# Optimization experiments

Hardware: AMD Instinct MI355X
Metric: run time of the kernel (lower is better)

## Reference

```python
import jax, jax.numpy as jnp
import numpy as np


def setup_inputs() -> dict:
    key = jax.random.key(0)
    ks = jax.random.split(key, 8)
    B, M, C, H, W = 2, 16, 256, 64, 64
    T = 1024  # transformer_dim
    return {
        "transformer_output": jax.random.normal(ks[0], (B, T), dtype=jnp.float32),
        "residual_maps": jax.random.normal(ks[1], (B, M, C, H, W), dtype=jnp.float32),
        "Wq": jax.random.normal(ks[2], (C, T), dtype=jnp.float32) * 0.02,
        "bq": jnp.zeros((C,), dtype=jnp.float32),
        "Wk": jax.random.normal(ks[3], (C, C), dtype=jnp.float32) * 0.02,
        "bk": jnp.zeros((C,), dtype=jnp.float32),
        "Wv": jax.random.normal(ks[4], (C, C), dtype=jnp.float32) * 0.02,
        "bv": jnp.zeros((C,), dtype=jnp.float32),
    }


def reference(transformer_output, residual_maps, Wq, bq, Wk, bk, Wv, bv):
    # residual_maps: [B, M, C, H, W]; single query per batch element.
    B, M, C, H, W = residual_maps.shape
    scale = C ** (-0.5)
    # Linear query projection: [B, C]
    q = transformer_output @ Wq.T + bq
    # 1x1 conv == per-pixel channel matmul: [B, M, C, H, W]
    keys = jnp.einsum("oc,bmchw->bmohw", Wk, residual_maps) + bk[None, None, :, None, None]
    values = jnp.einsum("oc,bmchw->bmohw", Wv, residual_maps) + bv[None, None, :, None, None]
    # Single-query dot-product scores per (map, pixel): [B, M, H, W]
    scores = jnp.einsum("bc,bmchw->bmhw", q, keys) * scale
    # Temporal softmax over num_maps at each spatial position
    probs = jax.nn.softmax(scores, axis=1)
    # Softmax-weighted sum of value maps: [B, C, H, W]
    out = jnp.einsum("bmhw,bmchw->bchw", probs, values)
    return out
```

## Files before the change

kernel.cpp:

```cpp
#include <hip/hip_runtime.h>

#define SCALE 0.0625f

typedef __attribute__((ext_vector_type(4))) float f32x4;
typedef __attribute__((ext_vector_type(8))) short s16x8;

__device__ __forceinline__ unsigned short f2bf(float x) {
    unsigned u = __float_as_uint(x);
    u = u + 0x7FFF + ((u >> 16) & 1);
    return (unsigned short)(u >> 16);
}

__global__ __launch_bounds__(256) void prep1_kernel(
    const float* __restrict__ TO,
    const float* __restrict__ Wq,
    const float* __restrict__ bq,
    const float* __restrict__ Wv,
    float* __restrict__ qbuf,
    unsigned short* __restrict__ WvB)
{
    const int blk = blockIdx.x;
    const int t   = threadIdx.x;
    if (blk < 16) {
        const int b    = blk >> 3;
        const int rblk = blk & 7;
        const int wv = t >> 6, l = t & 63;
        const float4* Wq4 = (const float4*)Wq;
        const float4* TO4 = (const float4*)TO;
        for (int rr = 0; rr < 8; ++rr) {
            const int c = rblk * 32 + wv * 8 + rr;
            float acc = 0.f;
#pragma unroll
            for (int i = 0; i < 4; ++i) {
                float4 wq = Wq4[c * 256 + i * 64 + l];
                float4 tv = TO4[b * 256 + i * 64 + l];
                acc = fmaf(wq.x, tv.x, acc);
                acc = fmaf(wq.y, tv.y, acc);
                acc = fmaf(wq.z, tv.z, acc);
                acc = fmaf(wq.w, tv.w, acc);
            }
#pragma unroll
            for (int mask = 1; mask < 64; mask <<= 1)
                acc += __shfl_xor(acc, mask, 64);
            if (l == 0) qbuf[b * 256 + c] = acc + bq[c];
        }
    } else {
        const int idx = blk - 16;
#pragma unroll
        for (int i = 0; i < 4; ++i) {
            const int e = idx * 4096 + i * 1024 + t * 4;
            const float4 f = ((const float4*)Wv)[e >> 2];
            ushort4 o;
            o.x = f2bf(f.x); o.y = f2bf(f.y);
            o.z = f2bf(f.z); o.w = f2bf(f.w);
            *(ushort4*)(WvB + e) = o;
        }
    }
}

__global__ __launch_bounds__(256) void prep2_kernel(
    const float* __restrict__ qbuf,
    const float* __restrict__ Wk,
    float* __restrict__ qks)
{
    const int blk = blockIdx.x;
    const int t   = threadIdx.x;
    const int b = blk >> 3, j = blk & 7;
    const int col = t & 31, chunk = t >> 5;
    const int cp = j * 32 + col;
    float partial = 0.f;
#pragma unroll 8
    for (int cc = 0; cc < 32; ++cc) {
        const int c = chunk * 32 + cc;
        partial = fmaf(qbuf[b * 256 + c], Wk[c * 256 + cp], partial);
    }
    __shared__ float r2[8][32];
    r2[chunk][col] = partial;
    __syncthreads();
    if (t < 32) {
        float s = 0.f;
#pragma unroll
        for (int k = 0; k < 8; ++k) s += r2[k][t];
        qks[b * 256 + j * 32 + t] = SCALE * s;
    }
}

__global__ __launch_bounds__(256) void scores_kernel(
    const float* __restrict__ X,
    const float* __restrict__ qks,
    float* __restrict__ scores)
{
    const int blk = blockIdx.x;
    const int bm  = blk >> 4;
    const int px  = ((blk & 15) << 8) + threadIdx.x;
    const float* __restrict__ Xr = X + bm * 1048576 + px;
    const float* __restrict__ qr = qks + (bm >> 4) * 256;
    float s0 = 0.f, s1 = 0.f, s2 = 0.f, s3 = 0.f;
#pragma unroll 4
    for (int c = 0; c < 256; c += 4) {
        s0 = fmaf(qr[c + 0], Xr[(c + 0) * 4096], s0);
        s1 = fmaf(qr[c + 1], Xr[(c + 1) * 4096], s1);
        s2 = fmaf(qr[c + 2], Xr[(c + 2) * 4096], s2);
        s3 = fmaf(qr[c + 3], Xr[(c + 3) * 4096], s3);
    }
    scores[bm * 4096 + px] = (s0 + s1) + (s2 + s3);
}

__global__ __launch_bounds__(256) void wxconv_kernel(
    const float* __restrict__ X,
    const float* __restrict__ scores,
    const unsigned short* __restrict__ WvB,
    const float* __restrict__ bv,
    float* __restrict__ out)
{
    const int t   = threadIdx.x;
    const int blk = blockIdx.x;
    const int pb  = ((blk & 7) << 6) | (blk >> 3);
    const int b   = pb >> 8;
    const int hw0 = (pb & 255) << 4;

    __shared__ float pl[16][16];
    __shared__ float invl[16];
    __shared__ float slab[256 * 20];

    {
        const int px_s = t & 15, m_s = t >> 4;
        const float e = __expf(scores[(b * 16 + m_s) * 4096 + hw0 + px_s]);
        pl[m_s][px_s] = e;
        __syncthreads();
        if (t < 16) {
            float s = 0.f;
#pragma unroll
            for (int m = 0; m < 16; ++m) s += pl[m][t];
            invl[t] = 1.0f / s;
        }
        __syncthreads();
        pl[m_s][px_s] *= invl[px_s];
        __syncthreads();
    }

    const int p4 = t & 3;
    const int cg = t >> 2;
    const float4* X4 = (const float4*)X;
    const int base0 = (b * 16) * 262144 + (hw0 >> 2) + p4;

    float4 v[2][4];
    float4 wx[4];
#pragma unroll
    for (int k = 0; k < 4; ++k) wx[k] = make_float4(0.f, 0.f, 0.f, 0.f);

#pragma unroll
    for (int k = 0; k < 4; ++k)
        v[0][k] = X4[base0 + (cg + 64 * k) * 1024];
    float4 pm[2];
    pm[0] = *(const float4*)&pl[0][4 * p4];

#pragma unroll
    for (int m = 0; m < 16; ++m) {
        const int buf = m & 1, nxt = buf ^ 1;
        if (m < 15) {
#pragma unroll
            for (int k = 0; k < 4; ++k)
                v[nxt][k] = X4[base0 + (m + 1) * 262144 + (cg + 64 * k) * 1024];
            pm[nxt] = *(const float4*)&pl[m + 1][4 * p4];
        }
#pragma unroll
        for (int k = 0; k < 4; ++k) {
            wx[k].x = fmaf(pm[buf].x, v[buf][k].x, wx[k].x);
            wx[k].y = fmaf(pm[buf].y, v[buf][k].y, wx[k].y);
            wx[k].z = fmaf(pm[buf].z, v[buf][k].z, wx[k].z);
            wx[k].w = fmaf(pm[buf].w, v[buf][k].w, wx[k].w);
        }
    }

#pragma unroll
    for (int k = 0; k < 4; ++k)
        *(float4*)&slab[(cg + 64 * k) * 20 + 4 * p4] = wx[k];
    __syncthreads();

    const int w    = t >> 6;
    const int lane = t & 63;
    const int px   = lane & 15;
    const int quad = lane >> 4;

    f32x4 acc[4];
#pragma unroll
    for (int i = 0; i < 4; ++i) {
        const int tt = 4 * w + i;
#pragma unroll
        for (int r = 0; r < 4; ++r)
            acc[i][r] = bv[16 * tt + quad * 4 + r];
    }

#pragma unroll
    for (int ks = 0; ks < 8; ++ks) {
        s16x8 bfr;
#pragma unroll
        for (int j = 0; j < 8; ++j)
            bfr[j] = (short)f2bf(slab[(ks * 32 + quad * 8 + j) * 20 + px]);
#pragma unroll
        for (int i = 0; i < 4; ++i) {
            const int tt = 4 * w + i;
            const s16x8 afr =
                *(const s16x8*)(WvB + (16 * tt + px) * 256 + ks * 32 + quad * 8);
            acc[i] = __builtin_amdgcn_mfma_f32_16x16x32_bf16(afr, bfr, acc[i],
                                                             0, 0, 0);
        }
    }

    const int obase = b * 1048576 + hw0;
#pragma unroll
    for (int i = 0; i < 4; ++i) {
        const int tt = 4 * w + i;
#pragma unroll
        for (int r = 0; r < 4; ++r) {
            const int co = 16 * tt + quad * 4 + r;
            out[obase + co * 4096 + px] = acc[i][r];
        }
    }
}

extern "C" void kernel_launch(void* const* d_in, const int* in_sizes, int n_in,
                              void* d_out, int out_size, void* d_ws, size_t ws_size,
                              hipStream_t stream) {
    const float* TO = (const float*)d_in[0];
    const float* X  = (const float*)d_in[1];
    const float* Wq = (const float*)d_in[2];
    const float* bq = (const float*)d_in[3];
    const float* Wk = (const float*)d_in[4];
    const float* Wv = (const float*)d_in[6];
    const float* bv = (const float*)d_in[7];
    float* out = (float*)d_out;
    float* ws  = (float*)d_ws;

    float*          qbuf   = ws;
    float*          qks    = ws + 512;
    unsigned short* WvB    = (unsigned short*)(ws + 1024);
    float*          scores = ws + 1024 + 32768;

    hipLaunchKernelGGL(prep1_kernel, dim3(32), dim3(256), 0, stream,
                       TO, Wq, bq, Wv, qbuf, WvB);
    hipLaunchKernelGGL(prep2_kernel, dim3(16), dim3(256), 0, stream,
                       qbuf, Wk, qks);
    hipLaunchKernelGGL(scores_kernel, dim3(512), dim3(256), 0, stream,
                       X, qks, scores);
    hipLaunchKernelGGL(wxconv_kernel, dim3(512), dim3(256), 0, stream,
                       X, scores, WvB, bv, out);
}
```

Baseline: 251.0 us.

## Fuse score computation into weighted-conv kernel with 32-pixel tiles

```diff
diff --git a/kernel.cpp b/kernel.cpp
--- a/kernel.cpp
+++ b/kernel.cpp
@@ -85,66 +85,59 @@
     }
 }
 
-__global__ __launch_bounds__(256) void scores_kernel(
+__global__ __launch_bounds__(512, 1) void fused_kernel(
     const float* __restrict__ X,
     const float* __restrict__ qks,
-    float* __restrict__ scores)
-{
-    const int blk = blockIdx.x;
-    const int bm  = blk >> 4;
-    const int px  = ((blk & 15) << 8) + threadIdx.x;
-    const float* __restrict__ Xr = X + bm * 1048576 + px;
-    const float* __restrict__ qr = qks + (bm >> 4) * 256;
-    float s0 = 0.f, s1 = 0.f, s2 = 0.f, s3 = 0.f;
-#pragma unroll 4
-    for (int c = 0; c < 256; c += 4) {
-        s0 = fmaf(qr[c + 0], Xr[(c + 0) * 4096], s0);
-        s1 = fmaf(qr[c + 1], Xr[(c + 1) * 4096], s1);
-        s2 = fmaf(qr[c + 2], Xr[(c + 2) * 4096], s2);
-        s3 = fmaf(qr[c + 3], Xr[(c + 3) * 4096], s3);
-    }
-    scores[bm * 4096 + px] = (s0 + s1) + (s2 + s3);
-}
-
-__global__ __launch_bounds__(256) void wxconv_kernel(
-    const float* __restrict__ X,
-    const float* __restrict__ scores,
     const unsigned short* __restrict__ WvB,
     const float* __restrict__ bv,
     float* __restrict__ out)
 {
     const int t   = threadIdx.x;
     const int blk = blockIdx.x;
-    const int pb  = ((blk & 7) << 6) | (blk >> 3);
-    const int b   = pb >> 8;
-    const int hw0 = (pb & 255) << 4;
-
-    __shared__ float pl[16][16];
-    __shared__ float invl[16];
-    __shared__ float slab[256 * 20];
+    const int b   = blk >> 7;
+    const int hw0 = (blk & 127) << 5;
+
+    __shared__ float pl[16][32];
+    __shared__ float invl[32];
+    __shared__ float slab[256 * 36];
 
     {
-        const int px_s = t & 15, m_s = t >> 4;
-        const float e = __expf(scores[(b * 16 + m_s) * 4096 + hw0 + px_s]);
-        pl[m_s][px_s] = e;
+        const int px = t & 31, ms = t >> 5;
+        const float* __restrict__ Xr = X + ((b * 16 + ms) * 256) * 4096 + hw0 + px;
+        const float* __restrict__ qr = qks + b * 256;
+        float a0 = 0.f, a1 = 0.f, a2 = 0.f, a3 = 0.f;
+        float a4 = 0.f, a5 = 0.f, a6 = 0.f, a7 = 0.f;
+#pragma unroll 4
+        for (int c = 0; c < 256; c += 8) {
+            a0 = fmaf(qr[c + 0], Xr[(c + 0) * 4096], a0);
+            a1 = fmaf(qr[c + 1], Xr[(c + 1) * 4096], a1);
+            a2 = fmaf(qr[c + 2], Xr[(c + 2) * 4096], a2);
+            a3 = fmaf(qr[c + 3], Xr[(c + 3) * 4096], a3);
+            a4 = fmaf(qr[c + 4], Xr[(c + 4) * 4096], a4);
+            a5 = fmaf(qr[c + 5], Xr[(c + 5) * 4096], a5);
+            a6 = fmaf(qr[c + 6], Xr[(c + 6) * 4096], a6);
+            a7 = fmaf(qr[c + 7], Xr[(c + 7) * 4096], a7);
+        }
+        const float s = ((a0 + a1) + (a2 + a3)) + ((a4 + a5) + (a6 + a7));
+        pl[ms][px] = __expf(s);
         __syncthreads();
-        if (t < 16) {
-            float s = 0.f;
-#pragma unroll
-            for (int m = 0; m < 16; ++m) s += pl[m][t];
-            invl[t] = 1.0f / s;
+        if (t < 32) {
+            float sm = 0.f;
+#pragma unroll
+            for (int m = 0; m < 16; ++m) sm += pl[m][t];
+            invl[t] = 1.0f / sm;
         }
         __syncthreads();
-        pl[m_s][px_s] *= invl[px_s];
+        pl[ms][px] *= invl[px];
         __syncthreads();
     }
 
-    const int p4 = t & 3;
-    const int cg = t >> 2;
+    const int p4 = t & 7;
+    const int cg = t >> 3;
     const float4* X4 = (const float4*)X;
     const int base0 = (b * 16) * 262144 + (hw0 >> 2) + p4;
 
-    float4 v[2][4];
+    float4 v[3][4];
     float4 wx[4];
 #pragma unroll
     for (int k = 0; k < 4; ++k) wx[k] = make_float4(0.f, 0.f, 0.f, 0.f);
@@ -152,41 +145,46 @@
 #pragma unroll
     for (int k = 0; k < 4; ++k)
         v[0][k] = X4[base0 + (cg + 64 * k) * 1024];
-    float4 pm[2];
-    pm[0] = *(const float4*)&pl[0][4 * p4];
+#pragma unroll
+    for (int k = 0; k < 4; ++k)
+        v[1][k] = X4[base0 + 262144 + (cg + 64 * k) * 1024];
 
 #pragma unroll
     for (int m = 0; m < 16; ++m) {
-        const int buf = m & 1, nxt = buf ^ 1;
-        if (m < 15) {
+        const int cur = m % 3;
+        const int nxt = (m + 2) % 3;
+        if (m < 14) {
 #pragma unroll
             for (int k = 0; k < 4; ++k)
-                v[nxt][k] = X4[base0 + (m + 1) * 262144 + (cg + 64 * k) * 1024];
-            pm[nxt] = *(const float4*)&pl[m + 1][4 * p4];
-        }
+                v[nxt][k] = X4[base0 + (m + 2) * 262144 + (cg + 64 * k) * 1024];
+        }
+        const float4 pm = *(const float4*)&pl[m][4 * p4];
 #pragma unroll
         for (int k = 0; k < 4; ++k) {
-            wx[k].x = fmaf(pm[buf].x, v[buf][k].x, wx[k].x);
-            wx[k].y = fmaf(pm[buf].y, v[buf][k].y, wx[k].y);
-            wx[k].z = fmaf(pm[buf].z, v[buf][k].z, wx[k].z);
-            wx[k].w = fmaf(pm[buf].w, v[buf][k].w, wx[k].w);
+            wx[k].x = fmaf(pm.x, v[cur][k].x, wx[k].x);
+            wx[k].y = fmaf(pm.y, v[cur][k].y, wx[k].y);
+            wx[k].z = fmaf(pm.z, v[cur][k].z, wx[k].z);
+            wx[k].w = fmaf(pm.w, v[cur][k].w, wx[k].w);
         }
     }
 
 #pragma unroll
     for (int k = 0; k < 4; ++k)
-        *(float4*)&slab[(cg + 64 * k) * 20 + 4 * p4] = wx[k];
+        *(float4*)&slab[(cg + 64 * k) * 36 + 4 * p4] = wx[k];
     __syncthreads();
 
     const int w    = t >> 6;
+    const int ph   = w & 1;
+    const int cot  = w >> 1;
     const int lane = t & 63;
-    const int px   = lane & 15;
+    const int pxl  = lane & 15;
     const int quad = lane >> 4;
+    const int px   = 16 * ph + pxl;
 
     f32x4 acc[4];
 #pragma unroll
     for (int i = 0; i < 4; ++i) {
-        const int tt = 4 * w + i;
+        const int tt = 4 * cot + i;
 #pragma unroll
         for (int r = 0; r < 4; ++r)
             acc[i][r] = bv[16 * tt + quad * 4 + r];
@@ -197,12 +195,12 @@
         s16x8 bfr;
 #pragma unroll
         for (int j = 0; j < 8; ++j)
-            bfr[j] = (short)f2bf(slab[(ks * 32 + quad * 8 + j) * 20 + px]);
+            bfr[j] = (short)f2bf(slab[(ks * 32 + quad * 8 + j) * 36 + px]);
 #pragma unroll
         for (int i = 0; i < 4; ++i) {
-            const int tt = 4 * w + i;
+            const int tt = 4 * cot + i;
             const s16x8 afr =
-                *(const s16x8*)(WvB + (16 * tt + px) * 256 + ks * 32 + quad * 8);
+                *(const s16x8*)(WvB + (16 * tt + pxl) * 256 + ks * 32 + quad * 8);
             acc[i] = __builtin_amdgcn_mfma_f32_16x16x32_bf16(afr, bfr, acc[i],
                                                              0, 0, 0);
         }
@@ -211,7 +209,7 @@
     const int obase = b * 1048576 + hw0;
 #pragma unroll
     for (int i = 0; i < 4; ++i) {
-        const int tt = 4 * w + i;
+        const int tt = 4 * cot + i;
 #pragma unroll
         for (int r = 0; r < 4; ++r) {
             const int co = 16 * tt + quad * 4 + r;
@@ -233,17 +231,14 @@
     float* out = (float*)d_out;
     float* ws  = (float*)d_ws;
 
-    float*          qbuf   = ws;
-    float*          qks    = ws + 512;
-    unsigned short* WvB    = (unsigned short*)(ws + 1024);
-    float*          scores = ws + 1024 + 32768;
+    float*          qbuf = ws;
+    float*          qks  = ws + 512;
+    unsigned short* WvB  = (unsigned short*)(ws + 1024);
 
     hipLaunchKernelGGL(prep1_kernel, dim3(32), dim3(256), 0, stream,
                        TO, Wq, bq, Wv, qbuf, WvB);
     hipLaunchKernelGGL(prep2_kernel, dim3(16), dim3(256), 0, stream,
                        qbuf, Wk, qks);
-    hipLaunchKernelGGL(scores_kernel, dim3(512), dim3(256), 0, stream,
-                       X, qks, scores);
-    hipLaunchKernelGGL(wxconv_kernel, dim3(512), dim3(256), 0, stream,
-                       X, scores, WvB, bv, out);
-}
+    hipLaunchKernelGGL(fused_kernel, dim3(256), dim3(512), 0, stream,
+                       X, qks, WvB, bv, out);
+}
```

New measurement: 249.2 us. No clear change (-0.7%).

## Split score reduction across channel chunks and add separate softmax kernel

Applied to the files above, without the earlier changes.

```diff
diff --git a/kernel.cpp b/kernel.cpp
--- a/kernel.cpp
+++ b/kernel.cpp
@@ -88,27 +88,72 @@
 __global__ __launch_bounds__(256) void scores_kernel(
     const float* __restrict__ X,
     const float* __restrict__ qks,
-    float* __restrict__ scores)
-{
-    const int blk = blockIdx.x;
-    const int bm  = blk >> 4;
+    float* __restrict__ part)
+{
+    const int blk = blockIdx.x;
+    const int bm  = blk >> 6;
+    const int cs  = (blk >> 2) & 15;
+    const int pxq = blk & 3;
+    const int b   = bm >> 4;
+    const int t   = threadIdx.x;
+
+    const float4* __restrict__ Xr =
+        (const float4*)X + bm * 262144 + cs * 16384 + pxq * 256 + t;
+    const float* __restrict__ qr = qks + b * 256 + cs * 16;
+
+    float4 a0 = {0,0,0,0}, a1 = {0,0,0,0}, a2 = {0,0,0,0}, a3 = {0,0,0,0};
+#pragma unroll
+    for (int j = 0; j < 16; j += 4) {
+        const float4 x0 = Xr[(j + 0) * 1024];
+        const float4 x1 = Xr[(j + 1) * 1024];
+        const float4 x2 = Xr[(j + 2) * 1024];
+        const float4 x3 = Xr[(j + 3) * 1024];
+        const float q0 = qr[j + 0], q1 = qr[j + 1];
+        const float q2 = qr[j + 2], q3 = qr[j + 3];
+        a0.x = fmaf(q0, x0.x, a0.x); a0.y = fmaf(q0, x0.y, a0.y);
+        a0.z = fmaf(q0, x0.z, a0.z); a0.w = fmaf(q0, x0.w, a0.w);
+        a1.x = fmaf(q1, x1.x, a1.x); a1.y = fmaf(q1, x1.y, a1.y);
+        a1.z = fmaf(q1, x1.z, a1.z); a1.w = fmaf(q1, x1.w, a1.w);
+        a2.x = fmaf(q2, x2.x, a2.x); a2.y = fmaf(q2, x2.y, a2.y);
+        a2.z = fmaf(q2, x2.z, a2.z); a2.w = fmaf(q2, x2.w, a2.w);
+        a3.x = fmaf(q3, x3.x, a3.x); a3.y = fmaf(q3, x3.y, a3.y);
+        a3.z = fmaf(q3, x3.z, a3.z); a3.w = fmaf(q3, x3.w, a3.w);
+    }
+    float4 s;
+    s.x = (a0.x + a1.x) + (a2.x + a3.x);
+    s.y = (a0.y + a1.y) + (a2.y + a3.y);
+    s.z = (a0.z + a1.z) + (a2.z + a3.z);
+    s.w = (a0.w + a1.w) + (a2.w + a3.w);
+    ((float4*)part)[(cs * 32 + bm) * 1024 + pxq * 256 + t] = s;
+}
+
+__global__ __launch_bounds__(256) void softmax_kernel(
+    const float* __restrict__ part,
+    float* __restrict__ probs)
+{
+    const int blk = blockIdx.x;
+    const int b   = blk >> 4;
     const int px  = ((blk & 15) << 8) + threadIdx.x;
-    const float* __restrict__ Xr = X + bm * 1048576 + px;
-    const float* __restrict__ qr = qks + (bm >> 4) * 256;
-    float s0 = 0.f, s1 = 0.f, s2 = 0.f, s3 = 0.f;
-#pragma unroll 4
-    for (int c = 0; c < 256; c += 4) {
-        s0 = fmaf(qr[c + 0], Xr[(c + 0) * 4096], s0);
-        s1 = fmaf(qr[c + 1], Xr[(c + 1) * 4096], s1);
-        s2 = fmaf(qr[c + 2], Xr[(c + 2) * 4096], s2);
-        s3 = fmaf(qr[c + 3], Xr[(c + 3) * 4096], s3);
-    }
-    scores[bm * 4096 + px] = (s0 + s1) + (s2 + s3);
-}
-
-__global__ __launch_bounds__(256) void wxconv_kernel(
+    float e[16];
+    float tot = 0.f;
+#pragma unroll
+    for (int m = 0; m < 16; ++m) {
+        float s = 0.f;
+#pragma unroll
+        for (int cc = 0; cc < 16; ++cc)
+            s += part[(cc * 32 + b * 16 + m) * 4096 + px];
+        e[m] = __expf(s);
+        tot += e[m];
+    }
+    const float inv = 1.0f / tot;
+#pragma unroll
+    for (int m = 0; m < 16; ++m)
+        probs[(b * 16 + m) * 4096 + px] = e[m] * inv;
+}
+
+__global__ __launch_bounds__(512, 1) void wxconv_kernel(
     const float* __restrict__ X,
-    const float* __restrict__ scores,
+    const float* __restrict__ probs,
     const unsigned short* __restrict__ WvB,
     const float* __restrict__ bv,
     float* __restrict__ out)
@@ -120,73 +165,74 @@
     const int hw0 = (pb & 255) << 4;
 
     __shared__ float pl[16][16];
-    __shared__ float invl[16];
     __shared__ float slab[256 * 20];
 
-    {
-        const int px_s = t & 15, m_s = t >> 4;
-        const float e = __expf(scores[(b * 16 + m_s) * 4096 + hw0 + px_s]);
-        pl[m_s][px_s] = e;
-        __syncthreads();
-        if (t < 16) {
-            float s = 0.f;
-#pragma unroll
-            for (int m = 0; m < 16; ++m) s += pl[m][t];
-            invl[t] = 1.0f / s;
-        }
-        __syncthreads();
-        pl[m_s][px_s] *= invl[px_s];
-        __syncthreads();
-    }
-
-    const int p4 = t & 3;
-    const int cg = t >> 2;
+    if (t < 256)
+        pl[t >> 4][t & 15] = probs[(b * 16 + (t >> 4)) * 4096 + hw0 + (t & 15)];
+    __syncthreads();
+
+    const int g    = t >> 8;
+    const int tl   = t & 255;
+    const int p4   = tl & 3;
+    const int cg   = tl >> 2;
+    const int m0   = g * 8;
+
     const float4* X4 = (const float4*)X;
-    const int base0 = (b * 16) * 262144 + (hw0 >> 2) + p4;
+    const int base = b * 16 * 262144 + (hw0 >> 2) + p4;
+
+    float4 wx[4];
+#pragma unroll
+    for (int k = 0; k < 4; ++k) wx[k] = make_float4(0.f, 0.f, 0.f, 0.f);
 
     float4 v[2][4];
-    float4 wx[4];
-#pragma unroll
-    for (int k = 0; k < 4; ++k) wx[k] = make_float4(0.f, 0.f, 0.f, 0.f);
-
 #pragma unroll
     for (int k = 0; k < 4; ++k)
-        v[0][k] = X4[base0 + (cg + 64 * k) * 1024];
-    float4 pm[2];
-    pm[0] = *(const float4*)&pl[0][4 * p4];
-
-#pragma unroll
-    for (int m = 0; m < 16; ++m) {
-        const int buf = m & 1, nxt = buf ^ 1;
-        if (m < 15) {
+        v[0][k] = X4[base + m0 * 262144 + (cg + 64 * k) * 1024];
+
+#pragma unroll
+    for (int mm = 0; mm < 8; ++mm) {
+        const int buf = mm & 1, nxt = buf ^ 1;
+        if (mm < 7) {
 #pragma unroll
             for (int k = 0; k < 4; ++k)
-                v[nxt][k] = X4[base0 + (m + 1) * 262144 + (cg + 64 * k) * 1024];
-            pm[nxt] = *(const float4*)&pl[m + 1][4 * p4];
-        }
+                v[nxt][k] = X4[base + (m0 + mm + 1) * 262144 + (cg + 64 * k) * 1024];
+        }
+        const float4 pm = *(const float4*)&pl[m0 + mm][4 * p4];
 #pragma unroll
         for (int k = 0; k < 4; ++k) {
-            wx[k].x = fmaf(pm[buf].x, v[buf][k].x, wx[k].x);
-            wx[k].y = fmaf(pm[buf].y, v[buf][k].y, wx[k].y);
-            wx[k].z = fmaf(pm[buf].z, v[buf][k].z, wx[k].z);
-            wx[k].w = fmaf(pm[buf].w, v[buf][k].w, wx[k].w);
-        }
-    }
-
-#pragma unroll
-    for (int k = 0; k < 4; ++k)
-        *(float4*)&slab[(cg + 64 * k) * 20 + 4 * p4] = wx[k];
+            wx[k].x = fmaf(pm.x, v[buf][k].x, wx[k].x);
+            wx[k].y = fmaf(pm.y, v[buf][k].y, wx[k].y);
+            wx[k].z = fmaf(pm.z, v[buf][k].z, wx[k].z);
+            wx[k].w = fmaf(pm.w, v[buf][k].w, wx[k].w);
+        }
+    }
+
+    if (g == 0) {
+#pragma unroll
+        for (int k = 0; k < 4; ++k)
+            *(float4*)&slab[(cg + 64 * k) * 20 + 4 * p4] = wx[k];
+    }
+    __syncthreads();
+    if (g == 1) {
+#pragma unroll
+        for (int k = 0; k < 4; ++k) {
+            float4* p = (float4*)&slab[(cg + 64 * k) * 20 + 4 * p4];
+            float4 s = *p;
+            s.x += wx[k].x; s.y += wx[k].y; s.z += wx[k].z; s.w += wx[k].w;
+            *p = s;
+        }
+    }
     __syncthreads();
 
     const int w    = t >> 6;
     const int lane = t & 63;
-    const int px   = lane & 15;
+    const int pxl  = lane & 15;
     const int quad = lane >> 4;
 
-    f32x4 acc[4];
-#pragma unroll
-    for (int i = 0; i < 4; ++i) {
-        const int tt = 4 * w + i;
+    f32x4 acc[2];
+#pragma unroll
+    for (int i = 0; i < 2; ++i) {
+        const int tt = 2 * w + i;
 #pragma unroll
         for (int r = 0; r < 4; ++r)
             acc[i][r] = bv[16 * tt + quad * 4 + r];
@@ -197,12 +243,12 @@
         s16x8 bfr;
 #pragma unroll
         for (int j = 0; j < 8; ++j)
-            bfr[j] = (short)f2bf(slab[(ks * 32 + quad * 8 + j) * 20 + px]);
-#pragma unroll
-        for (int i = 0; i < 4; ++i) {
-            const int tt = 4 * w + i;
+            bfr[j] = (short)f2bf(slab[(ks * 32 + quad * 8 + j) * 20 + pxl]);
+#pragma unroll
+        for (int i = 0; i < 2; ++i) {
+            const int tt = 2 * w + i;
             const s16x8 afr =
-                *(const s16x8*)(WvB + (16 * tt + px) * 256 + ks * 32 + quad * 8);
+                *(const s16x8*)(WvB + (16 * tt + pxl) * 256 + ks * 32 + quad * 8);
             acc[i] = __builtin_amdgcn_mfma_f32_16x16x32_bf16(afr, bfr, acc[i],
                                                              0, 0, 0);
         }
@@ -210,12 +256,12 @@
 
     const int obase = b * 1048576 + hw0;
 #pragma unroll
-    for (int i = 0; i < 4; ++i) {
-        const int tt = 4 * w + i;
+    for (int i = 0; i < 2; ++i) {
+        const int tt = 2 * w + i;
 #pragma unroll
         for (int r = 0; r < 4; ++r) {
             const int co = 16 * tt + quad * 4 + r;
-            out[obase + co * 4096 + px] = acc[i][r];
+            out[obase + co * 4096 + pxl] = acc[i][r];
         }
     }
 }
@@ -233,17 +279,20 @@
     float* out = (float*)d_out;
     float* ws  = (float*)d_ws;
 
-    float*          qbuf   = ws;
-    float*          qks    = ws + 512;
-    unsigned short* WvB    = (unsigned short*)(ws + 1024);
-    float*          scores = ws + 1024 + 32768;
+    float*          qbuf  = ws;
+    float*          qks   = ws + 512;
+    unsigned short* WvB   = (unsigned short*)(ws + 1024);
+    float*          part  = ws + 33792;
+    float*          probs = ws + 33792 + 2097152;
 
     hipLaunchKernelGGL(prep1_kernel, dim3(32), dim3(256), 0, stream,
                        TO, Wq, bq, Wv, qbuf, WvB);
     hipLaunchKernelGGL(prep2_kernel, dim3(16), dim3(256), 0, stream,
                        qbuf, Wk, qks);
-    hipLaunchKernelGGL(scores_kernel, dim3(512), dim3(256), 0, stream,
-                       X, qks, scores);
-    hipLaunchKernelGGL(wxconv_kernel, dim3(512), dim3(256), 0, stream,
-                       X, scores, WvB, bv, out);
-}
+    hipLaunchKernelGGL(scores_kernel, dim3(2048), dim3(256), 0, stream,
+                       X, qks, part);
+    hipLaunchKernelGGL(softmax_kernel, dim3(32), dim3(256), 0, stream,
+                       part, probs);
+    hipLaunchKernelGGL(wxconv_kernel, dim3(512), dim3(512), 0, stream,
+                       X, probs, WvB, bv, out);
+}
```

After: 317.5 us. +26.5%, slower.
